# Kernel optimization log

Hardware: AMD Instinct MI355X
Metric: run time of the kernel (lower is better)

## Reference

```python
import jax, jax.numpy as jnp
import numpy as np

N, C, T, V, D = 128, 64, 256, 25, 64  # batch(*persons), in_ch, frames, joints, out_ch
RED = 4  # SE reduction


def _shift_indices(c, d, v):
    i = np.arange(v)[:, None]
    j = np.arange(c)[None, :]
    shift_in = ((i * c + j + j * c) % (c * v)).reshape(-1)
    jd = np.arange(d)[None, :]
    shift_out = ((i * d + jd - jd * d) % (d * v)).reshape(-1)
    return jnp.asarray(shift_in, jnp.int32), jnp.asarray(shift_out, jnp.int32)


def setup_inputs() -> dict:
    key = jax.random.key(0)
    ks = jax.random.split(key, 6)
    r = C // RED
    x0 = jax.random.normal(ks[0], (N, C, T, V), jnp.float32)
    fc1_w = jax.random.normal(ks[1], (r, C), jnp.float32) * (2.0 / C) ** 0.5
    fc1_b = jnp.zeros((r,), jnp.float32)
    fc2_w = jax.random.normal(ks[2], (4, r), jnp.float32) * (2.0 / r) ** 0.5
    fc2_b = jnp.zeros((4,), jnp.float32)
    W = jax.random.normal(ks[3], (4, C, D), jnp.float32) * (1.0 / D) ** 0.5
    b = jnp.zeros((4, D), jnp.float32)
    mask = jax.random.normal(ks[4], (1, V, C), jnp.float32) * 0.1  # Feature_Mask
    gamma = jnp.ones((V * D,), jnp.float32)
    beta = jnp.zeros((V * D,), jnp.float32)
    shift_in, shift_out = _shift_indices(C, D, V)
    return dict(x0=x0, epoch=100, fc1_w=fc1_w, fc1_b=fc1_b, fc2_w=fc2_w,
                fc2_b=fc2_b, W=W, b=b, mask=mask, gamma=gamma, beta=beta,
                shift_in=shift_in, shift_out=shift_out)


def reference(x0, epoch, fc1_w, fc1_b, fc2_w, fc2_b, W, b, mask, gamma, beta,
              shift_in, shift_out):
    n, c, t, v = x0.shape
    d = W.shape[-1]
    # DY_SEModule: global avg pool -> 1x1 conv -> relu -> 1x1 conv -> softmax(/tao)
    pooled = x0.mean(axis=(2, 3))                       # [n, c]
    h = jax.nn.relu(pooled @ fc1_w.T + fc1_b)           # [n, c//4]
    logits = h @ fc2_w.T + fc2_b                        # [n, 4]
    tao = 1.0 if epoch >= 60 else -(30.0 - 1.0) / 60.0 * epoch + 30.0
    gate = jax.nn.softmax(logits / tao, axis=1)         # [n, 4]
    # per-sample fused weights/bias
    Wf = jnp.einsum('kcd,nk->ncd', W, gate)             # [n, c, d]
    bf = jnp.einsum('kc,nk->nc', b, gate)               # [n, d]
    # shift-in gather + tanh feature mask
    x = x0.transpose(0, 2, 3, 1).reshape(n * t, v * c)  # [n*t, v*c]
    x = jnp.take(x, shift_in, axis=1).reshape(n * t, v, c)
    x = x * (jnp.tanh(mask) + 1.0)
    x = x.reshape(n, t, v, c)
    # per-sample linear
    x = jnp.einsum('ntvc,ncd->ntvd', x, Wf) + bf[:, None, None, :]
    # shift-out gather + BatchNorm1d over v*d features (training-mode stats)
    x = jnp.take(x.reshape(n * t, v * d), shift_out, axis=1)
    mu = x.mean(axis=0)
    var = x.var(axis=0)
    x = (x - mu) * jax.lax.rsqrt(var + 1e-5) * gamma + beta
    x = x.reshape(n, t, v, d).transpose(0, 3, 1, 2)     # [n, d, t, v]
    # residual (in==out -> identity down) + relu
    return jax.nn.relu(x + x0)
```

## Files before the change

kernel.cpp:

```cpp
#include <hip/hip_runtime.h>
#include <hip/hip_bf16.h>
#include <math.h>

#define N_   128
#define C_   64
#define T_   256
#define V_   25
#define D_   64
#define CTV  409600
#define TV   6400

typedef __attribute__((ext_vector_type(8))) short short8;
typedef __attribute__((ext_vector_type(4))) short short4v;
typedef __attribute__((ext_vector_type(4))) float f32x4;

__device__ inline unsigned short f2b(float f) {
    __hip_bfloat16 h = __float2bfloat16(f);
    return *(unsigned short*)&h;
}
__device__ inline float b2f(unsigned short u) {
    return __uint_as_float(((unsigned)u) << 16);
}

__global__ __launch_bounds__(256) void k_pool(const float* __restrict__ x0,
                                              float* __restrict__ pooled) {
    const int bid = blockIdx.x;
    const int tid = threadIdx.x;
    const float4* base = (const float4*)(x0 + (size_t)bid * TV);
    float s = 0.f;
    for (int i = tid; i < 1600; i += 256) {
        float4 f = base[i];
        s += (f.x + f.y) + (f.z + f.w);
    }
    #pragma unroll
    for (int off = 32; off > 0; off >>= 1) s += __shfl_down(s, off);
    __shared__ float red[4];
    if ((tid & 63) == 0) red[tid >> 6] = s;
    __syncthreads();
    if (tid == 0) pooled[bid] = (red[0] + red[1] + red[2] + red[3]) * (1.0f / TV);
}

__global__ __launch_bounds__(256) void k_se(
    const float* __restrict__ pooled, const float* __restrict__ fc1w,
    const float* __restrict__ fc1b,  const float* __restrict__ fc2w,
    const float* __restrict__ fc2b,  const float* __restrict__ Wm,
    const float* __restrict__ bm,    const float* __restrict__ mask,
    const int* __restrict__ ep,
    unsigned short* __restrict__ Wfb, float* __restrict__ bfv,
    unsigned* __restrict__ mgp)
{
    __shared__ float sp[64], sh[16], sl[4];
    __shared__ float wk[64 * 65];
    const int tid = threadIdx.x, n = blockIdx.x;
    if (tid < 64) sp[tid] = pooled[n * 64 + tid];
    __syncthreads();
    if (tid < 16) {
        float s = fc1b[tid];
        #pragma unroll
        for (int c = 0; c < 64; c++) s = fmaf(sp[c], fc1w[tid * 64 + c], s);
        sh[tid] = fmaxf(s, 0.f);
    }
    __syncthreads();
    if (tid < 4) {
        float s = fc2b[tid];
        #pragma unroll
        for (int j = 0; j < 16; j++) s = fmaf(sh[j], fc2w[tid * 16 + j], s);
        sl[tid] = s;
    }
    __syncthreads();
    const int e = ep[0];
    const float tao = (e >= 60) ? 1.0f : (-(29.0f / 60.0f) * (float)e + 30.0f);
    const float it = 1.0f / tao;
    float l0 = sl[0] * it, l1 = sl[1] * it, l2 = sl[2] * it, l3 = sl[3] * it;
    float mx = fmaxf(fmaxf(l0, l1), fmaxf(l2, l3));
    float e0 = expf(l0 - mx), e1 = expf(l1 - mx), e2 = expf(l2 - mx), e3 = expf(l3 - mx);
    float inv = 1.0f / (e0 + e1 + e2 + e3);
    float ga[4] = {e0 * inv, e1 * inv, e2 * inv, e3 * inv};

    float accW[16];
    #pragma unroll
    for (int m = 0; m < 16; m++) accW[m] = 0.f;
    #pragma unroll
    for (int k = 0; k < 4; k++) {
        __syncthreads();
        for (int i = tid; i < 4096; i += 256)
            wk[(i >> 6) * 65 + (i & 63)] = Wm[k * 4096 + i];
        __syncthreads();
        #pragma unroll
        for (int m = 0; m < 16; m++) {
            int o = m * 256 + tid;
            int w  = o >> 10, s = (o >> 9) & 1;
            int ln = (o >> 3) & 63, j = o & 7;
            int c  = s * 32 + (ln >> 4) * 8 + j;
            int d  = w * 16 + (ln & 15);
            accW[m] = fmaf(ga[k], wk[c * 65 + d], accW[m]);
        }
    }
    #pragma unroll
    for (int m = 0; m < 16; m++)
        Wfb[(size_t)n * 4096 + m * 256 + tid] = f2b(accW[m]);
    if (tid < 64)
        bfv[n * 64 + tid] = ga[0] * bm[tid] + ga[1] * bm[64 + tid] +
                            ga[2] * bm[128 + tid] + ga[3] * bm[192 + tid];
    if (n == 0) {
        for (int j2 = tid; j2 < 800; j2 += 256) {
            int v = j2 >> 5, c = (j2 & 31) * 2;
            unsigned m0 = (unsigned)f2b(tanhf(mask[v * 64 + c]) + 1.0f);
            unsigned m1 = (unsigned)f2b(tanhf(mask[v * 64 + c + 1]) + 1.0f);
            mgp[j2] = (m1 << 16) | m0;
        }
    }
}

__global__ __launch_bounds__(256, 4) void k_main(
    const float* __restrict__ x0, const unsigned short* __restrict__ Wfb,
    const float* __restrict__ bfv, const unsigned* __restrict__ mgp,
    __hip_bfloat16* __restrict__ y, float* __restrict__ sn)
{
    __shared__ unsigned short xs[6400];
    __shared__ unsigned short At[7616];
    __shared__ unsigned mgS[800];

    const int tid = threadIdx.x;
    const int w = tid >> 6, l = tid & 63, q = l >> 4, m = l & 15;
    const int n = blockIdx.x >> 4;
    const int tbase = (blockIdx.x & 15) * 16;

    short8 bf0 = *(const short8*)(Wfb + (size_t)n * 4096 + (w * 2 + 0) * 512 + l * 8);
    short8 bf1 = *(const short8*)(Wfb + (size_t)n * 4096 + (w * 2 + 1) * 512 + l * 8);
    const int d = w * 16 + m;
    const float bfl = bfv[n * 64 + d];

    for (int i = tid; i < 800; i += 256) mgS[i] = mgp[i];
    for (int i = tid; i < 408; i += 256) {
        int rr = i / 34, wo = i - rr * 34;
        int t = rr / 3, vr = rr - t * 3 + 1;
        ((unsigned*)At)[(96 + t * 4 + vr) * 34 + wo] = 0u;
    }

    float ss[25], sq[25];
    #pragma unroll
    for (int v = 0; v < 25; v++) { ss[v] = 0.f; sq[v] = 0.f; }

    for (int sub = 0; sub < 4; sub++) {
        const int t0 = tbase + sub * 4;
        __syncthreads();
        {
            const float4* src = (const float4*)x0;
            const int fb = n * 102400 + (t0 * 25) / 4;
            for (int i = tid; i < 1600; i += 256) {
                int c = i / 25, r = i - c * 25;
                float4 f = src[fb + c * 1600 + r];
                unsigned lo = ((unsigned)f2b(f.y) << 16) | f2b(f.x);
                unsigned hi = ((unsigned)f2b(f.w) << 16) | f2b(f.z);
                *(unsigned*)&xs[c * 100 + r * 4]     = lo;
                *(unsigned*)&xs[c * 100 + r * 4 + 2] = hi;
            }
        }
        __syncthreads();
        for (int p = tid; p < 3200; p += 256) {
            int cp = p & 31, rv = p >> 5;
            int t = rv / 25, v = rv - t * 25;
            int c = cp * 2;
            unsigned mg = mgS[v * 32 + cp];
            int v0 = (v + c) % 25;
            int v1 = v0 + 1; if (v1 == 25) v1 = 0;
            float x0v = b2f(xs[c * 100 + t * 25 + v0])       * b2f((unsigned short)(mg & 0xffff));
            float x1v = b2f(xs[(c + 1) * 100 + t * 25 + v1]) * b2f((unsigned short)(mg >> 16));
            int rho = (v >> 2) * 16 + t * 4 + (v & 3);
            *(unsigned*)&At[rho * 68 + c] = ((unsigned)f2b(x1v) << 16) | f2b(x0v);
        }
        __syncthreads();
        #pragma unroll
        for (int tau = 0; tau < 7; tau++) {
            const unsigned short* Ab = At + (tau * 16 + m) * 68 + q * 8;
            short4v a0l = *(const short4v*)(Ab);
            short4v a0h = *(const short4v*)(Ab + 4);
            short4v a1l = *(const short4v*)(Ab + 32);
            short4v a1h = *(const short4v*)(Ab + 36);
            short8 a0 = {a0l[0],a0l[1],a0l[2],a0l[3],a0h[0],a0h[1],a0h[2],a0h[3]};
            short8 a1 = {a1l[0],a1l[1],a1l[2],a1l[3],a1h[0],a1h[1],a1h[2],a1h[3]};
            f32x4 acc = {0.f, 0.f, 0.f, 0.f};
            acc = __builtin_amdgcn_mfma_f32_16x16x32_bf16(a0, bf0, acc, 0, 0, 0);
            acc = __builtin_amdgcn_mfma_f32_16x16x32_bf16(a1, bf1, acc, 0, 0, 0);
            const int t = t0 + q;
            __hip_bfloat16* yb = y + ((size_t)(n * T_ + t) * 25) * 64 + d;
            #pragma unroll
            for (int r = 0; r < 4; r++) {
                const int v = tau * 4 + r;
                if (v < 25) {
                    float val = acc[r] + bfl;
                    yb[v * 64] = __float2bfloat16(val);
                    ss[v] += val;
                    sq[v] = fmaf(val, val, sq[v]);
                }
            }
        }
    }
    #pragma unroll
    for (int v = 0; v < 25; v++) {
        ss[v] += __shfl_xor(ss[v], 16); ss[v] += __shfl_xor(ss[v], 32);
        sq[v] += __shfl_xor(sq[v], 16); sq[v] += __shfl_xor(sq[v], 32);
    }
    if (q == 0) {
        float* sb = sn + (size_t)n * 3200;
        #pragma unroll
        for (int v = 0; v < 25; v++) {
            atomicAdd(&sb[v * 64 + d], ss[v]);
            atomicAdd(&sb[1600 + v * 64 + d], sq[v]);
        }
    }
}

__global__ __launch_bounds__(256) void k_bn(
    const float* __restrict__ sn,
    const float* __restrict__ gamma, const float* __restrict__ beta,
    const int* __restrict__ shout,
    float2* __restrict__ ab)
{
    const int tid = threadIdx.x;
    const int jl = tid >> 2;
    const int p  = tid & 3;
    const int j = blockIdx.x * 64 + jl;
    const int src = shout[j];
    float s = 0.f, qq = 0.f;
    for (int nn = p; nn < 128; nn += 4) {
        s  += sn[(size_t)nn * 3200 + src];
        qq += sn[(size_t)nn * 3200 + 1600 + src];
    }
    s  += __shfl_xor(s, 1);  s  += __shfl_xor(s, 2);
    qq += __shfl_xor(qq, 1); qq += __shfl_xor(qq, 2);
    if (p == 0) {
        const float invn = 1.0f / 32768.0f;
        float mu = s * invn;
        float var = qq * invn - mu * mu;
        float rstd = rsqrtf(var + 1e-5f);
        float a = gamma[j] * rstd;
        float bb = beta[j] - mu * a;
        int dd = j & 63, vo = j >> 6;
        ab[dd * 25 + vo] = make_float2(a, bb);
    }
}

__global__ __launch_bounds__(256, 7) void k_out(
    const __hip_bfloat16* __restrict__ y, const float* __restrict__ x0,
    const float2* __restrict__ ab, float* __restrict__ out)
{
    __shared__ __align__(16) unsigned short ys[4 * 1652];
    const int tid = threadIdx.x;
    const int n = blockIdx.x >> 6;
    const int t0 = (blockIdx.x & 63) * 4;
    const uint4* ysrc = (const uint4*)((const unsigned short*)y + (size_t)(n * T_ + t0) * 1600);
    for (int i = tid; i < 800; i += 256) {
        uint4 g = ysrc[i];
        int tl = i / 200, r8 = (i - tl * 200) * 8;
        int v = r8 >> 6, d0 = r8 & 63;
        unsigned* p = (unsigned*)ys + ((tl * 1652 + v * 66 + d0) >> 1);
        p[0] = g.x; p[1] = g.y; p[2] = g.z; p[3] = g.w;
    }
    __syncthreads();
    const float* xb = x0 + (size_t)n * CTV + t0 * 25;
    float* ob = out + (size_t)n * CTV + t0 * 25;
    for (int o4 = tid; o4 < 1600; o4 += 256) {
        int dd = o4 / 25;
        int rem4 = (o4 - dd * 25) * 4;
        int ddm = dd;
        if (ddm >= 25) ddm -= 25;
        if (ddm >= 25) ddm -= 25;
        int tl = rem4 / 25, vo = rem4 - tl * 25;
        const int base = dd * TV + rem4;
        f32x4 xv = __builtin_nontemporal_load((const f32x4*)(xb + base));
        f32x4 r;
        #pragma unroll
        for (int e = 0; e < 4; e++) {
            int vy = vo - ddm; if (vy < 0) vy += 25;
            float val = b2f(ys[tl * 1652 + vy * 66 + dd]);
            float2 g = ab[dd * 25 + vo];
            r[e] = fmaxf(fmaf(val, g.x, g.y) + xv[e], 0.f);
            vo++; if (vo == 25) { vo = 0; tl++; }
        }
        __builtin_nontemporal_store(r, (f32x4*)(ob + base));
    }
}

extern "C" void kernel_launch(void* const* d_in, const int* in_sizes, int n_in,
                              void* d_out, int out_size, void* d_ws, size_t ws_size,
                              hipStream_t stream) {
    const float* x0    = (const float*)d_in[0];
    const int*   ep    = (const int*)  d_in[1];
    const float* fc1w  = (const float*)d_in[2];
    const float* fc1b  = (const float*)d_in[3];
    const float* fc2w  = (const float*)d_in[4];
    const float* fc2b  = (const float*)d_in[5];
    const float* Wm    = (const float*)d_in[6];
    const float* bm    = (const float*)d_in[7];
    const float* mask  = (const float*)d_in[8];
    const float* gamma = (const float*)d_in[9];
    const float* beta  = (const float*)d_in[10];
    const int*   shout = (const int*)  d_in[12];
    float* out = (float*)d_out;

    float* wsf = (float*)d_ws;
    float*          pooled = wsf;
    float*          bfv    = wsf + 8192;
    unsigned*       mgp    = (unsigned*)(wsf + 16384);
    float2*         ab     = (float2*)(wsf + 17984);
    unsigned short* Wfb    = (unsigned short*)(wsf + 22784);
    float*          sn     = wsf + 284928;
    __hip_bfloat16* y      = (__hip_bfloat16*)(wsf + 694528);

    hipMemsetAsync(sn, 0, 409600 * sizeof(float), stream);
    k_pool<<<N_ * C_, 256, 0, stream>>>(x0, pooled);
    k_se<<<N_, 256, 0, stream>>>(pooled, fc1w, fc1b, fc2w, fc2b, Wm, bm, mask,
                                 ep, Wfb, bfv, mgp);
    k_main<<<N_ * 16, 256, 0, stream>>>(x0, Wfb, bfv, mgp, y, sn);
    k_bn<<<25, 256, 0, stream>>>(sn, gamma, beta, shout, ab);
    k_out<<<N_ * 64, 256, 0, stream>>>(y, x0, ab, out);
}
```

Measured before the change: 589.5 us.

## Precompute bf16 x slab in pool kernel and async-load it in main kernel

The pool kernel now also writes a bf16 copy of x0, laid out in contiguous per-chunk slabs. The main kernel fills its shared-memory tile directly with global_load_lds (direct global-to-LDS copies), and prefetches the next sub-tile while the MFMA stage runs, instead of converting fp32 x0 in registers each iteration. This halves the bytes the main kernel reads and removes the conversion work from its critical path, at the cost of an extra bf16 write of x0 in the pool kernel. The output kernel is also retiled to 8 frames per block with 8 elements per thread, and its x0 reads switch from nontemporal to plain loads.

```diff
diff --git a/kernel.cpp b/kernel.cpp
--- a/kernel.cpp
+++ b/kernel.cpp
@@ -14,6 +14,11 @@
 typedef __attribute__((ext_vector_type(4))) short short4v;
 typedef __attribute__((ext_vector_type(4))) float f32x4;
 
+typedef __attribute__((address_space(1))) unsigned uag;
+typedef __attribute__((address_space(3))) unsigned ual;
+#define GLD16(gp, lp) __builtin_amdgcn_global_load_lds( \
+    (uag*)(unsigned long long)(gp), (ual*)(unsigned)(unsigned long long)(lp), 16, 0, 0)
+
 __device__ inline unsigned short f2b(float f) {
     __hip_bfloat16 h = __float2bfloat16(f);
     return *(unsigned short*)&h;
@@ -23,14 +28,21 @@
 }
 
 __global__ __launch_bounds__(256) void k_pool(const float* __restrict__ x0,
-                                              float* __restrict__ pooled) {
+                                              float* __restrict__ pooled,
+                                              unsigned short* __restrict__ xb16) {
     const int bid = blockIdx.x;
     const int tid = threadIdx.x;
+    const int n = bid >> 6, c = bid & 63;
     const float4* base = (const float4*)(x0 + (size_t)bid * TV);
     float s = 0.f;
     for (int i = tid; i < 1600; i += 256) {
         float4 f = base[i];
         s += (f.x + f.y) + (f.z + f.w);
+        int flat = i * 4;
+        int chunk = flat / 100;
+        int within = flat - chunk * 100;
+        short4v pk = { (short)f2b(f.x), (short)f2b(f.y), (short)f2b(f.z), (short)f2b(f.w) };
+        *(short4v*)(xb16 + ((size_t)((n * 64 + chunk) * 64 + c)) * 100 + within) = pk;
     }
     #pragma unroll
     for (int off = 32; off > 0; off >>= 1) s += __shfl_down(s, off);
@@ -113,11 +125,11 @@
 }
 
 __global__ __launch_bounds__(256, 4) void k_main(
-    const float* __restrict__ x0, const unsigned short* __restrict__ Wfb,
+    const unsigned short* __restrict__ xb16, const unsigned short* __restrict__ Wfb,
     const float* __restrict__ bfv, const unsigned* __restrict__ mgp,
     __hip_bfloat16* __restrict__ y, float* __restrict__ sn)
 {
-    __shared__ unsigned short xs[6400];
+    __shared__ __align__(16) unsigned short xs[6400];
     __shared__ unsigned short At[7616];
     __shared__ unsigned mgS[800];
 
@@ -125,6 +137,7 @@
     const int w = tid >> 6, l = tid & 63, q = l >> 4, m = l & 15;
     const int n = blockIdx.x >> 4;
     const int tbase = (blockIdx.x & 15) * 16;
+    const int chunk0 = (blockIdx.x & 15) * 4;
 
     short8 bf0 = *(const short8*)(Wfb + (size_t)n * 4096 + (w * 2 + 0) * 512 + l * 8);
     short8 bf1 = *(const short8*)(Wfb + (size_t)n * 4096 + (w * 2 + 1) * 512 + l * 8);
@@ -137,6 +150,11 @@
         int t = rr / 3, vr = rr - t * 3 + 1;
         ((unsigned*)At)[(96 + t * 4 + vr) * 34 + wo] = 0u;
     }
+    {
+        const unsigned short* slab = xb16 + (size_t)(n * 64 + chunk0) * 6400;
+        for (int i = tid; i < 800; i += 256)
+            GLD16((const unsigned*)slab + i * 4, (unsigned*)xs + i * 4);
+    }
 
     float ss[25], sq[25];
     #pragma unroll
@@ -144,19 +162,6 @@
 
     for (int sub = 0; sub < 4; sub++) {
         const int t0 = tbase + sub * 4;
-        __syncthreads();
-        {
-            const float4* src = (const float4*)x0;
-            const int fb = n * 102400 + (t0 * 25) / 4;
-            for (int i = tid; i < 1600; i += 256) {
-                int c = i / 25, r = i - c * 25;
-                float4 f = src[fb + c * 1600 + r];
-                unsigned lo = ((unsigned)f2b(f.y) << 16) | f2b(f.x);
-                unsigned hi = ((unsigned)f2b(f.w) << 16) | f2b(f.z);
-                *(unsigned*)&xs[c * 100 + r * 4]     = lo;
-                *(unsigned*)&xs[c * 100 + r * 4 + 2] = hi;
-            }
-        }
         __syncthreads();
         for (int p = tid; p < 3200; p += 256) {
             int cp = p & 31, rv = p >> 5;
@@ -171,6 +176,11 @@
             *(unsigned*)&At[rho * 68 + c] = ((unsigned)f2b(x1v) << 16) | f2b(x0v);
         }
         __syncthreads();
+        if (sub < 3) {
+            const unsigned short* slab = xb16 + (size_t)(n * 64 + chunk0 + sub + 1) * 6400;
+            for (int i = tid; i < 800; i += 256)
+                GLD16((const unsigned*)slab + i * 4, (unsigned*)xs + i * 4);
+        }
         #pragma unroll
         for (int tau = 0; tau < 7; tau++) {
             const unsigned short* Ab = At + (tau * 16 + m) * 68 + q * 8;
@@ -242,16 +252,16 @@
     }
 }
 
-__global__ __launch_bounds__(256, 7) void k_out(
+__global__ __launch_bounds__(256, 6) void k_out(
     const __hip_bfloat16* __restrict__ y, const float* __restrict__ x0,
     const float2* __restrict__ ab, float* __restrict__ out)
 {
-    __shared__ __align__(16) unsigned short ys[4 * 1652];
+    __shared__ __align__(16) unsigned short ys[8 * 1652];
     const int tid = threadIdx.x;
-    const int n = blockIdx.x >> 6;
-    const int t0 = (blockIdx.x & 63) * 4;
+    const int n = blockIdx.x >> 5;
+    const int t0 = (blockIdx.x & 31) * 8;
     const uint4* ysrc = (const uint4*)((const unsigned short*)y + (size_t)(n * T_ + t0) * 1600);
-    for (int i = tid; i < 800; i += 256) {
+    for (int i = tid; i < 1600; i += 256) {
         uint4 g = ysrc[i];
         int tl = i / 200, r8 = (i - tl * 200) * 8;
         int v = r8 >> 6, d0 = r8 & 63;
@@ -261,25 +271,28 @@
     __syncthreads();
     const float* xb = x0 + (size_t)n * CTV + t0 * 25;
     float* ob = out + (size_t)n * CTV + t0 * 25;
-    for (int o4 = tid; o4 < 1600; o4 += 256) {
-        int dd = o4 / 25;
-        int rem4 = (o4 - dd * 25) * 4;
+    for (int o8 = tid; o8 < 1600; o8 += 256) {
+        int dd = o8 / 25;
+        int rem8 = (o8 - dd * 25) * 8;
         int ddm = dd;
         if (ddm >= 25) ddm -= 25;
         if (ddm >= 25) ddm -= 25;
-        int tl = rem4 / 25, vo = rem4 - tl * 25;
-        const int base = dd * TV + rem4;
-        f32x4 xv = __builtin_nontemporal_load((const f32x4*)(xb + base));
-        f32x4 r;
-        #pragma unroll
-        for (int e = 0; e < 4; e++) {
+        int tl = rem8 / 25, vo = rem8 - tl * 25;
+        const int base = dd * TV + rem8;
+        f32x4 xv0 = *(const f32x4*)(xb + base);
+        f32x4 xv1 = *(const f32x4*)(xb + base + 4);
+        f32x4 r0, r1;
+        #pragma unroll
+        for (int e = 0; e < 8; e++) {
             int vy = vo - ddm; if (vy < 0) vy += 25;
             float val = b2f(ys[tl * 1652 + vy * 66 + dd]);
             float2 g = ab[dd * 25 + vo];
-            r[e] = fmaxf(fmaf(val, g.x, g.y) + xv[e], 0.f);
+            float rr = fmaxf(fmaf(val, g.x, g.y) + ((e < 4) ? xv0[e] : xv1[e - 4]), 0.f);
+            if (e < 4) r0[e] = rr; else r1[e - 4] = rr;
             vo++; if (vo == 25) { vo = 0; tl++; }
         }
-        __builtin_nontemporal_store(r, (f32x4*)(ob + base));
+        __builtin_nontemporal_store(r0, (f32x4*)(ob + base));
+        __builtin_nontemporal_store(r1, (f32x4*)(ob + base + 4));
     }
 }
 
@@ -308,12 +321,13 @@
     unsigned short* Wfb    = (unsigned short*)(wsf + 22784);
     float*          sn     = wsf + 284928;
     __hip_bfloat16* y      = (__hip_bfloat16*)(wsf + 694528);
+    unsigned short* xb16   = (unsigned short*)(wsf + 26908928);
 
     hipMemsetAsync(sn, 0, 409600 * sizeof(float), stream);
-    k_pool<<<N_ * C_, 256, 0, stream>>>(x0, pooled);
+    k_pool<<<N_ * C_, 256, 0, stream>>>(x0, pooled, xb16);
     k_se<<<N_, 256, 0, stream>>>(pooled, fc1w, fc1b, fc2w, fc2b, Wm, bm, mask,
                                  ep, Wfb, bfv, mgp);
-    k_main<<<N_ * 16, 256, 0, stream>>>(x0, Wfb, bfv, mgp, y, sn);
+    k_main<<<N_ * 16, 256, 0, stream>>>(xb16, Wfb, bfv, mgp, y, sn);
     k_bn<<<25, 256, 0, stream>>>(sn, gamma, beta, shout, ab);
-    k_out<<<N_ * 64, 256, 0, stream>>>(y, x0, ab, out);
-}
+    k_out<<<N_ * 32, 256, 0, stream>>>(y, x0, ab, out);
+}
```

New measurement: 611.3 us. +3.7%, slower.
